# Kernel tuning notes

Hardware: AMD Instinct MI355X
Metric: run time of the kernel (lower is better)

Reference implementation:

```python
import jax, jax.numpy as jnp
import numpy as np

N = 512          # pedestrians in scene
T = 12           # decode steps
OBS = 8
FEAT = 2
LAT = 32
COND = 64
LSTM_IN = 128
HID = 64         # lstm_hidden_size == context_state_size
CTX = 64
EMB = 32         # Pooling_net spatial embedding dim
MLP_IN = EMB + 2 * CTX   # 160
MLP_MID = 64
BOT = CTX        # bottleneck_dim = h_dim
IN_DEC = COND + LAT + CTX + FEAT  # 162


def setup_inputs() -> dict:
    key = jax.random.key(0)
    ks = jax.random.split(key, 24)
    s = 0.1
    return {
        "last_position": jax.random.normal(ks[0], (N, FEAT), jnp.float32),
        "c": jax.random.normal(ks[1], (N, COND), jnp.float32),
        "z": jax.random.normal(ks[2], (N, LAT), jnp.float32),
        "obs_traj_pos": jax.random.normal(ks[3], (OBS, N, FEAT), jnp.float32),
        "nei_index": jax.random.randint(ks[4], (T, N, N), 0, 2, jnp.int32),
        "nei_num_index": jax.random.randint(ks[5], (N,), 0, N, jnp.int32),
        "h0": jax.random.normal(ks[6], (N, HID), jnp.float32),
        "c0": jax.random.normal(ks[7], (N, HID), jnp.float32),
        "eps": jax.random.normal(ks[8], (T, N, FEAT), jnp.float32),
        "W_in": jax.random.normal(ks[9], (IN_DEC, LSTM_IN), jnp.float32) * s,
        "b_in": jnp.zeros((LSTM_IN,), jnp.float32),
        "W_ih": jax.random.normal(ks[10], (4 * HID, LSTM_IN), jnp.float32) * s,
        "W_hh": jax.random.normal(ks[11], (4 * HID, HID), jnp.float32) * s,
        "b_ih": jnp.zeros((4 * HID,), jnp.float32),
        "b_hh": jnp.zeros((4 * HID,), jnp.float32),
        "W_l2p": jax.random.normal(ks[12], (HID // 2 + CTX, FEAT), jnp.float32) * s,
        "b_l2p": jnp.zeros((FEAT,), jnp.float32),
        "W_sp": jax.random.normal(ks[13], (FEAT, EMB), jnp.float32) * s,
        "b_sp": jnp.zeros((EMB,), jnp.float32),
        "W1": jax.random.normal(ks[14], (MLP_IN, MLP_MID), jnp.float32) * s,
        "b1": jnp.zeros((MLP_MID,), jnp.float32),
        "W2": jax.random.normal(ks[15], (MLP_MID, BOT), jnp.float32) * s,
        "b2": jnp.zeros((BOT,), jnp.float32),
    }


def reference(last_position, c, z, obs_traj_pos, nei_index, nei_num_index,
              h0, c0, eps, W_in, b_in, W_ih, W_hh, b_ih, b_hh,
              W_l2p, b_l2p, W_sp, b_sp, W1, b1, W2, b2):
    sg = jax.lax.stop_gradient
    half = HID // 2
    neg_inf = jnp.float32(-jnp.inf)

    def pooling(mask, lstm_state, pos):
        # mask: [N,N] bool; lstm_state: [N,CTX]; pos: [N,2]
        corr = pos[:, None, :] - pos[None, :, :]           # [N,N,2] pos[i]-pos[j]
        r = corr @ W_sp + b_sp                              # [N,N,EMB]
        hj = jnp.broadcast_to(lstm_state[None, :, :], (N, N, CTX))
        hi = jnp.broadcast_to(lstm_state[:, None, :], (N, N, CTX))
        x = jnp.concatenate([r, hj, hi], axis=-1)           # [N,N,160]
        h1 = jax.nn.relu(x @ W1 + b1)
        h2 = jax.nn.relu(h1 @ W2 + b2)                      # [N,N,BOT]
        Hm = jnp.where(mask[:, :, None], h2, neg_inf)       # scatter of valid rows
        pool = Hm.max(axis=1)                               # max over neighbors j
        return jnp.where(pool == neg_inf, 0.0, pool)

    def lstm_cell(x, h, cs):
        gates = x @ W_ih.T + b_ih + h @ W_hh.T + b_hh
        i, f, g, o = jnp.split(gates, 4, axis=-1)
        c_new = jax.nn.sigmoid(f) * cs + jax.nn.sigmoid(i) * jnp.tanh(g)
        h_new = jax.nn.sigmoid(o) * jnp.tanh(c_new)
        return h_new, c_new

    def step(carry, xs):
        prev_pos, h, cs, ctx, cur_abs = carry
        nei_t, eps_t = xs
        emb = jnp.concatenate([sg(prev_pos), sg(c), sg(z), sg(ctx)], axis=-1)
        x = jax.nn.relu(emb @ W_in + b_in)
        h, cs = lstm_cell(x, h, cs)
        ctx = pooling(nei_t > 0, h, cur_abs)
        mu = jnp.concatenate([h[:, :half], ctx], -1) @ W_l2p + b_l2p
        logvar = jnp.concatenate([h[:, half:], ctx], -1) @ W_l2p + b_l2p
        pos = mu + eps_t * jnp.exp(0.5 * logvar)
        cur_abs = sg(cur_abs + pos)
        return (pos, h, cs, ctx, cur_abs), (pos, mu, logvar)

    ctx0 = jnp.zeros((N, CTX), jnp.float32)
    carry0 = (last_position, h0, c0, ctx0, obs_traj_pos[-1])
    _, (pre_pos, mean, var) = jax.lax.scan(step, carry0, (nei_index, eps))
    return pre_pos, mean, var
```

## Files before the change

### kernel.cpp

```cpp
#include <hip/hip_runtime.h>
#include <math.h>

#define NP 512
#define TT 12

typedef float f32x4 __attribute__((ext_vector_type(4)));
typedef __bf16 bf16x8 __attribute__((ext_vector_type(8)));

#define OFF_CURABS 0
#define OFF_QB     2048
#define OFF_P      34816
#define OFF_H      67584
#define OFF_CS     100352
#define OFF_XCZ    133120
#define OFF_WGB    198656
#define OFF_WCTXB  223232
#define OFF_W1B    227328
#define OFF_WIN01  231424
#define OFF_WC     231680
#define OFF_BASE   231808
#define OFF_W2F    231872

__global__ __launch_bounds__(256) void init_k(
    const float* __restrict__ obs, const float* __restrict__ cc,
    const float* __restrict__ zz,
    const float* __restrict__ W_in, const float* __restrict__ W_ih,
    const float* __restrict__ W_hh, const float* __restrict__ W_sp,
    const float* __restrict__ b_sp, const float* __restrict__ W1,
    const float* __restrict__ b1, const float* __restrict__ W2,
    float* __restrict__ ws) {
  if (blockIdx.x < 128) {
    int id = blockIdx.x * 256 + threadIdx.x;
    if (id < 1024) ws[OFF_CURABS + id] = obs[7 * 1024 + id];
    __bf16* wgb = (__bf16*)(ws + OFF_WGB);
    for (int e = id; e < 49152; e += 32768) {
      int k = e >> 8, g = e & 255;
      float v = (k < 128) ? W_ih[g * 128 + k] : W_hh[g * 64 + (k - 128)];
      wgb[e] = (__bf16)v;
    }
    if (id < 8192) {
      int d = id >> 7, k = id & 127;
      ((__bf16*)(ws + OFF_WCTXB))[id] = (__bf16)W_in[(98 + d) * 128 + k];
    }
    if (id < 8192) {
      int r = id >> 6, m = id & 63;
      ((__bf16*)(ws + OFF_W1B))[id] = (__bf16)W1[(32 + r) * 64 + m];
    }
    if (id < 256) ws[OFF_WIN01 + id] = W_in[(id >> 7) * 128 + (id & 127)];
    if (id < 128) {
      int d = id >> 6, m = id & 63;
      float s = 0.f;
      for (int e = 0; e < 32; ++e) s = fmaf(W_sp[d * 32 + e], W1[e * 64 + m], s);
      ws[OFF_WC + id] = s;
    }
    if (id < 64) {
      float s = b1[id];
      for (int e = 0; e < 32; ++e) s = fmaf(b_sp[e], W1[e * 64 + id], s);
      ws[OFF_BASE + id] = s;
    }
    if (id < 4096) {
      int e = id & 7, f = (id >> 3) & 7, cq = id >> 6;
      int col = cq >> 2, quad = cq & 3, mt = f >> 1, kh = f & 1;
      ((__bf16*)(ws + OFF_W2F))[id] =
          (__bf16)W2[(kh * 32 + quad * 8 + e) * 64 + (mt * 16 + col)];
    }
  } else {
    int b = blockIdx.x - 128;
    int k = threadIdx.x;
    if (k < 128) {
      float s = 0.f;
      for (int d = 0; d < 64; ++d) s = fmaf(cc[b * 64 + d], W_in[(2 + d) * 128 + k], s);
      for (int d = 0; d < 32; ++d) s = fmaf(zz[b * 32 + d], W_in[(66 + d) * 128 + k], s);
      ws[OFF_XCZ + b * 128 + k] = s;
    }
  }
}

__global__ __launch_bounds__(256) void step_k(
    const float* __restrict__ lastpos, const int* __restrict__ nei,
    const float* __restrict__ h0, const float* __restrict__ c0,
    const float* __restrict__ obs, const float* __restrict__ epsin,
    const float* __restrict__ b_in,
    const float* __restrict__ b_ih, const float* __restrict__ b_hh,
    const float* __restrict__ Wl2p, const float* __restrict__ bl2p,
    const float* __restrict__ b2,
    float* __restrict__ out, float* __restrict__ ws, int s) {
  __shared__ int   ml[512];
  __shared__ float wcl[128], basev[64];
  __shared__ float red[4][64];
  __shared__ float hloc[64], csloc[64], ctxloc[64], prevp[2], pxy[2];
  __shared__ float xpart[2][128], xvec[128], gl[256];

  int t = threadIdx.x;
  int b = blockIdx.x;
  int lane = t & 63, w = t >> 6;
  int quad = lane >> 4, col = lane & 15;

  float pf = 0.f;
  if (s < TT) {
    const float* wsrc = ws + OFF_WGB;
    #pragma unroll
    for (int k = 0; k < 4; ++k) pf += wsrc[(t + k * 256) * 24];
  }

  if (t < 64) {
    if (s == 0) { hloc[t] = h0[b * 64 + t]; csloc[t] = c0[b * 64 + t]; ctxloc[t] = 0.f; }
    else        { hloc[t] = ws[OFF_H + b * 64 + t]; csloc[t] = ws[OFF_CS + b * 64 + t]; }
    basev[t] = ws[OFF_BASE + t];
  } else if (t < 192) {
    wcl[t - 64] = ws[OFF_WC + (t - 64)];
  }
  if (s == 0 && t < 2) {
    prevp[t] = lastpos[b * 2 + t];
    pxy[t]   = obs[7 * 1024 + b * 2 + t];
  }
  if (s > 0) {
    const int* neirow = nei + ((size_t)(s - 1) * NP + b) * NP;
    for (int j = t; j < 512; j += 256) ml[j] = neirow[j];
  }
  if (pf == 1.2345e-33f) ws[OFF_CURABS + 1] = pf;
  __syncthreads();

  if (s > 0) {
    int st = s - 1;
    const __bf16* Qb = (const __bf16*)(ws + OFF_QB) + (st & 1) * 32768;
    const __bf16* wf = (const __bf16*)(ws + OFF_W2F) + (col * 4 + quad) * 64;
    bf16x8 bf00 = *(const bf16x8*)&wf[0];
    bf16x8 bf01 = *(const bf16x8*)&wf[8];
    bf16x8 bf10 = *(const bf16x8*)&wf[16];
    bf16x8 bf11 = *(const bf16x8*)&wf[24];
    bf16x8 bf20 = *(const bf16x8*)&wf[32];
    bf16x8 bf21 = *(const bf16x8*)&wf[40];
    bf16x8 bf30 = *(const bf16x8*)&wf[48];
    bf16x8 bf31 = *(const bf16x8*)&wf[56];
    float pl0[8], pl1[8];
    #pragma unroll
    for (int e = 0; e < 8; ++e) {
      pl0[e] = ws[OFF_P + b * 64 + quad * 8 + e];
      pl1[e] = ws[OFF_P + b * 64 + 32 + quad * 8 + e];
    }
    float vmax0 = -1e30f, vmax1 = -1e30f, vmax2 = -1e30f, vmax3 = -1e30f;

    for (int c = 0; c < 8; ++c) {
      int j = w * 128 + c * 16 + col;
      bf16x8 q0 = *(const bf16x8*)&Qb[j * 64 + quad * 8];
      bf16x8 q1 = *(const bf16x8*)&Qb[j * 64 + 32 + quad * 8];
      bf16x8 a0, a1;
      #pragma unroll
      for (int e = 0; e < 8; ++e) {
        a0[e] = (__bf16)fmaxf((float)q0[e] + pl0[e], 0.f);
        a1[e] = (__bf16)fmaxf((float)q1[e] + pl1[e], 0.f);
      }
      int mrow = w * 128 + c * 16 + quad * 4;
      bool mk0 = ml[mrow] > 0, mk1 = ml[mrow + 1] > 0,
           mk2 = ml[mrow + 2] > 0, mk3 = ml[mrow + 3] > 0;
      f32x4 acc;
      acc = (f32x4){0.f, 0.f, 0.f, 0.f};
      acc = __builtin_amdgcn_mfma_f32_16x16x32_bf16(a0, bf00, acc, 0, 0, 0);
      acc = __builtin_amdgcn_mfma_f32_16x16x32_bf16(a1, bf01, acc, 0, 0, 0);
      vmax0 = fmaxf(vmax0, mk0 ? acc[0] : -1e30f);
      vmax0 = fmaxf(vmax0, mk1 ? acc[1] : -1e30f);
      vmax0 = fmaxf(vmax0, mk2 ? acc[2] : -1e30f);
      vmax0 = fmaxf(vmax0, mk3 ? acc[3] : -1e30f);
      acc = (f32x4){0.f, 0.f, 0.f, 0.f};
      acc = __builtin_amdgcn_mfma_f32_16x16x32_bf16(a0, bf10, acc, 0, 0, 0);
      acc = __builtin_amdgcn_mfma_f32_16x16x32_bf16(a1, bf11, acc, 0, 0, 0);
      vmax1 = fmaxf(vmax1, mk0 ? acc[0] : -1e30f);
      vmax1 = fmaxf(vmax1, mk1 ? acc[1] : -1e30f);
      vmax1 = fmaxf(vmax1, mk2 ? acc[2] : -1e30f);
      vmax1 = fmaxf(vmax1, mk3 ? acc[3] : -1e30f);
      acc = (f32x4){0.f, 0.f, 0.f, 0.f};
      acc = __builtin_amdgcn_mfma_f32_16x16x32_bf16(a0, bf20, acc, 0, 0, 0);
      acc = __builtin_amdgcn_mfma_f32_16x16x32_bf16(a1, bf21, acc, 0, 0, 0);
      vmax2 = fmaxf(vmax2, mk0 ? acc[0] : -1e30f);
      vmax2 = fmaxf(vmax2, mk1 ? acc[1] : -1e30f);
      vmax2 = fmaxf(vmax2, mk2 ? acc[2] : -1e30f);
      vmax2 = fmaxf(vmax2, mk3 ? acc[3] : -1e30f);
      acc = (f32x4){0.f, 0.f, 0.f, 0.f};
      acc = __builtin_amdgcn_mfma_f32_16x16x32_bf16(a0, bf30, acc, 0, 0, 0);
      acc = __builtin_amdgcn_mfma_f32_16x16x32_bf16(a1, bf31, acc, 0, 0, 0);
      vmax3 = fmaxf(vmax3, mk0 ? acc[0] : -1e30f);
      vmax3 = fmaxf(vmax3, mk1 ? acc[1] : -1e30f);
      vmax3 = fmaxf(vmax3, mk2 ? acc[2] : -1e30f);
      vmax3 = fmaxf(vmax3, mk3 ? acc[3] : -1e30f);
    }
    vmax0 = fmaxf(vmax0, __shfl_xor(vmax0, 16));
    vmax0 = fmaxf(vmax0, __shfl_xor(vmax0, 32));
    vmax1 = fmaxf(vmax1, __shfl_xor(vmax1, 16));
    vmax1 = fmaxf(vmax1, __shfl_xor(vmax1, 32));
    vmax2 = fmaxf(vmax2, __shfl_xor(vmax2, 16));
    vmax2 = fmaxf(vmax2, __shfl_xor(vmax2, 32));
    vmax3 = fmaxf(vmax3, __shfl_xor(vmax3, 16));
    vmax3 = fmaxf(vmax3, __shfl_xor(vmax3, 32));
    if (lane < 16) {
      red[w][0 * 16 + lane] = vmax0;
      red[w][1 * 16 + lane] = vmax1;
      red[w][2 * 16 + lane] = vmax2;
      red[w][3 * 16 + lane] = vmax3;
    }
    __syncthreads();
    if (t < 64) {
      float m4 = fmaxf(fmaxf(red[0][t], red[1][t]),
                       fmaxf(red[2][t], red[3][t]));
      ctxloc[t] = fmaxf(m4 + b2[t], 0.f);
    }
    __syncthreads();
    if (t < 64) {
      int l = t;
      float cl = ctxloc[l];
      float sc0 = cl * Wl2p[(32 + l) * 2 + 0];
      float sc1 = cl * Wl2p[(32 + l) * 2 + 1];
      float m0 = 0.f, m1 = 0.f, v0 = 0.f, v1 = 0.f;
      if (l < 32) {
        float hm = hloc[l];
        m0 = hm * Wl2p[l * 2 + 0]; m1 = hm * Wl2p[l * 2 + 1];
        float hv = hloc[32 + l];
        v0 = hv * Wl2p[l * 2 + 0]; v1 = hv * Wl2p[l * 2 + 1];
      }
      for (int off = 32; off >= 1; off >>= 1) {
        sc0 += __shfl_down(sc0, off);
        sc1 += __shfl_down(sc1, off);
        m0  += __shfl_down(m0,  off);
        m1  += __shfl_down(m1,  off);
        v0  += __shfl_down(v0,  off);
        v1  += __shfl_down(v1,  off);
      }
      if (l == 0) {
        float mu0 = m0 + sc0 + bl2p[0], mu1 = m1 + sc1 + bl2p[1];
        float lv0 = v0 + sc0 + bl2p[0], lv1 = v1 + sc1 + bl2p[1];
        float e0 = epsin[st * 1024 + b * 2 + 0];
        float e1 = epsin[st * 1024 + b * 2 + 1];
        float p0 = mu0 + e0 * expf(0.5f * lv0);
        float p1 = mu1 + e1 * expf(0.5f * lv1);
        out[st * 1024 + b * 2 + 0] = p0;
        out[st * 1024 + b * 2 + 1] = p1;
        out[12288 + st * 1024 + b * 2 + 0] = mu0;
        out[12288 + st * 1024 + b * 2 + 1] = mu1;
        out[24576 + st * 1024 + b * 2 + 0] = lv0;
        out[24576 + st * 1024 + b * 2 + 1] = lv1;
        float px = ws[OFF_CURABS + (st & 1) * 1024 + b * 2 + 0];
        float py = ws[OFF_CURABS + (st & 1) * 1024 + b * 2 + 1];
        float nx = px + p0, ny = py + p1;
        ws[OFF_CURABS + ((st & 1) ^ 1) * 1024 + b * 2 + 0] = nx;
        ws[OFF_CURABS + ((st & 1) ^ 1) * 1024 + b * 2 + 1] = ny;
        pxy[0] = nx; pxy[1] = ny;
        prevp[0] = p0; prevp[1] = p1;
      }
    }
    __syncthreads();
  }

  if (s < TT) {
    {
      int k = t & 127, p = t >> 7;
      const __bf16* wctx = (const __bf16*)(ws + OFF_WCTXB);
      float a0 = 0.f, a1 = 0.f;
      if (p == 0)
        a0 = ws[OFF_XCZ + b * 128 + k] +
             prevp[0] * ws[OFF_WIN01 + k] + prevp[1] * ws[OFF_WIN01 + 128 + k];
      int d = p;
      for (; d + 2 < 64; d += 4) {
        a0 = fmaf(ctxloc[d],     (float)wctx[d * 128 + k],       a0);
        a1 = fmaf(ctxloc[d + 2], (float)wctx[(d + 2) * 128 + k], a1);
      }
      if (d < 64) a0 = fmaf(ctxloc[d], (float)wctx[d * 128 + k], a0);
      xpart[p][k] = a0 + a1;
    }
    __syncthreads();
    if (t < 128) xvec[t] = fmaxf(xpart[0][t] + xpart[1][t] + b_in[t], 0.f);
    __syncthreads();
    {
      int g = t;
      const __bf16* wgb = (const __bf16*)(ws + OFF_WGB);
      float s0 = 0.f, s1 = 0.f, s2 = 0.f, s3 = 0.f;
      for (int kk = 0; kk < 128; kk += 4) {
        s0 = fmaf(xvec[kk],     (float)wgb[kk * 256 + g],       s0);
        s1 = fmaf(xvec[kk + 1], (float)wgb[(kk + 1) * 256 + g], s1);
        s2 = fmaf(xvec[kk + 2], (float)wgb[(kk + 2) * 256 + g], s2);
        s3 = fmaf(xvec[kk + 3], (float)wgb[(kk + 3) * 256 + g], s3);
      }
      for (int kk = 0; kk < 64; kk += 4) {
        s0 = fmaf(hloc[kk],     (float)wgb[(128 + kk) * 256 + g], s0);
        s1 = fmaf(hloc[kk + 1], (float)wgb[(129 + kk) * 256 + g], s1);
        s2 = fmaf(hloc[kk + 2], (float)wgb[(130 + kk) * 256 + g], s2);
        s3 = fmaf(hloc[kk + 3], (float)wgb[(131 + kk) * 256 + g], s3);
      }
      gl[g] = b_ih[g] + b_hh[g] + ((s0 + s1) + (s2 + s3));
    }
    __syncthreads();
    if (t < 64) {
      float ig = gl[t], fg = gl[64 + t], gg = gl[128 + t], og = gl[192 + t];
      float is = 1.f / (1.f + expf(-ig));
      float fs = 1.f / (1.f + expf(-fg));
      float os = 1.f / (1.f + expf(-og));
      float cn = fs * csloc[t] + is * tanhf(gg);
      float hv = os * tanhf(cn);
      hloc[t] = hv;
      ws[OFF_CS + b * 64 + t] = cn;
      ws[OFF_H + b * 64 + t] = hv;
    }
    __syncthreads();
    if (t < 128) {
      int which = t >> 6, m = t & 63;
      const __bf16* wb = (const __bf16*)(ws + OFF_W1B) + which * 4096 + m;
      float s0 = 0.f, s1 = 0.f, s2 = 0.f, s3 = 0.f;
      for (int k = 0; k < 64; k += 4) {
        s0 = fmaf(hloc[k],     (float)wb[k * 64],       s0);
        s1 = fmaf(hloc[k + 1], (float)wb[(k + 1) * 64], s1);
        s2 = fmaf(hloc[k + 2], (float)wb[(k + 2) * 64], s2);
        s3 = fmaf(hloc[k + 3], (float)wb[(k + 3) * 64], s3);
      }
      float sv = (s0 + s1) + (s2 + s3);
      float cx = pxy[0], cy = pxy[1];
      if (which == 0)
        ((__bf16*)(ws + OFF_QB))[(s & 1) * 32768 + b * 64 + m] =
            (__bf16)(sv + basev[m] - cx * wcl[m] - cy * wcl[64 + m]);
      else
        ws[OFF_P + b * 64 + m] = sv + cx * wcl[m] + cy * wcl[64 + m];
    }
  }
}

extern "C" void kernel_launch(void* const* d_in, const int* in_sizes, int n_in,
                              void* d_out, int out_size, void* d_ws, size_t ws_size,
                              hipStream_t stream) {
  const float* lastpos = (const float*)d_in[0];
  const float* cc      = (const float*)d_in[1];
  const float* zz      = (const float*)d_in[2];
  const float* obs     = (const float*)d_in[3];
  const int*   nei     = (const int*)d_in[4];
  const float* h0      = (const float*)d_in[6];
  const float* c0      = (const float*)d_in[7];
  const float* eps     = (const float*)d_in[8];
  const float* W_in    = (const float*)d_in[9];
  const float* b_in    = (const float*)d_in[10];
  const float* W_ih    = (const float*)d_in[11];
  const float* W_hh    = (const float*)d_in[12];
  const float* b_ih    = (const float*)d_in[13];
  const float* b_hh    = (const float*)d_in[14];
  const float* W_l2p   = (const float*)d_in[15];
  const float* b_l2p   = (const float*)d_in[16];
  const float* W_sp    = (const float*)d_in[17];
  const float* b_sp    = (const float*)d_in[18];
  const float* W1      = (const float*)d_in[19];
  const float* b1      = (const float*)d_in[20];
  const float* W2      = (const float*)d_in[21];
  const float* b2      = (const float*)d_in[22];
  float* out = (float*)d_out;
  float* ws  = (float*)d_ws;

  hipLaunchKernelGGL(init_k, dim3(640), dim3(256), 0, stream,
                     obs, cc, zz, W_in, W_ih, W_hh, W_sp, b_sp, W1, b1, W2, ws);
  for (int s = 0; s <= TT; ++s) {
    hipLaunchKernelGGL(step_k, dim3(NP), dim3(256), 0, stream,
                       lastpos, nei, h0, c0, obs, eps,
                       b_in, b_ih, b_hh, W_l2p, b_l2p,
                       b2, out, ws, s);
  }
}
```

Before: 336.8 us.

## Replace per-step kernel launches with persistent kernel and global atomic barrier

Replaces 13 separate step launches with a single persistent kernel of 64 blocks, each owning 8 pedestrians, that keeps h, c, ctx and positions in shared memory and syncs across blocks with an atomic counter barrier per step. Weight layouts are transposed for vectorized bf16 reads, and the Q matrix is streamed through double-buffered LDS tiles. This removes launch overhead and global state round-trips. In exchange it uses only 64 CUs, so each block computes the pooling over all 512 neighbours for 8 pedestrians, and the spin barrier relies on all blocks being co-resident.

Result: slower. 721.5 us (+114.2%).

```diff
diff --git a/kernel.cpp b/kernel.cpp
--- a/kernel.cpp
+++ b/kernel.cpp
@@ -3,27 +3,29 @@
 
 #define NP 512
 #define TT 12
+#define NB 64
 
 typedef float f32x4 __attribute__((ext_vector_type(4)));
 typedef __bf16 bf16x8 __attribute__((ext_vector_type(8)));
 
-#define OFF_CURABS 0
-#define OFF_QB     2048
-#define OFF_P      34816
-#define OFF_H      67584
-#define OFF_CS     100352
-#define OFF_XCZ    133120
-#define OFF_WGB    198656
-#define OFF_WCTXB  223232
-#define OFF_W1B    227328
-#define OFF_WIN01  231424
-#define OFF_WC     231680
-#define OFF_BASE   231808
-#define OFF_W2F    231872
+#define OFF_QB     0
+#define OFF_XCZ    32768
+#define OFF_WGT    98304
+#define OFF_WCTXT  122880
+#define OFF_W1T    126976
+#define OFF_WIN01  131072
+#define OFF_WC     131328
+#define OFF_BASE   131456
+#define OFF_W2F    131520
+#define OFF_BAR    133568
+
+#define AT_LD64(p)   __hip_atomic_load((p), __ATOMIC_RELAXED, __HIP_MEMORY_SCOPE_AGENT)
+#define AT_ST32(p,v) __hip_atomic_store((p), (v), __ATOMIC_RELAXED, __HIP_MEMORY_SCOPE_AGENT)
+
+union BU { __bf16 h; unsigned short u; };
 
 __global__ __launch_bounds__(256) void init_k(
-    const float* __restrict__ obs, const float* __restrict__ cc,
-    const float* __restrict__ zz,
+    const float* __restrict__ cc, const float* __restrict__ zz,
     const float* __restrict__ W_in, const float* __restrict__ W_ih,
     const float* __restrict__ W_hh, const float* __restrict__ W_sp,
     const float* __restrict__ b_sp, const float* __restrict__ W1,
@@ -31,20 +33,18 @@
     float* __restrict__ ws) {
   if (blockIdx.x < 128) {
     int id = blockIdx.x * 256 + threadIdx.x;
-    if (id < 1024) ws[OFF_CURABS + id] = obs[7 * 1024 + id];
-    __bf16* wgb = (__bf16*)(ws + OFF_WGB);
+    __bf16* wgt = (__bf16*)(ws + OFF_WGT);
     for (int e = id; e < 49152; e += 32768) {
-      int k = e >> 8, g = e & 255;
-      float v = (k < 128) ? W_ih[g * 128 + k] : W_hh[g * 64 + (k - 128)];
-      wgb[e] = (__bf16)v;
+      int g = e / 192, k = e - g * 192;
+      wgt[e] = (__bf16)((k < 128) ? W_ih[g * 128 + k] : W_hh[g * 64 + (k - 128)]);
     }
     if (id < 8192) {
-      int d = id >> 7, k = id & 127;
-      ((__bf16*)(ws + OFF_WCTXB))[id] = (__bf16)W_in[(98 + d) * 128 + k];
+      int k = id >> 6, d = id & 63;
+      ((__bf16*)(ws + OFF_WCTXT))[id] = (__bf16)W_in[(98 + d) * 128 + k];
     }
     if (id < 8192) {
-      int r = id >> 6, m = id & 63;
-      ((__bf16*)(ws + OFF_W1B))[id] = (__bf16)W1[(32 + r) * 64 + m];
+      int which = id >> 12, m = (id >> 6) & 63, k = id & 63;
+      ((__bf16*)(ws + OFF_W1T))[id] = (__bf16)W1[(32 + which * 64 + k) * 64 + m];
     }
     if (id < 256) ws[OFF_WIN01 + id] = W_in[(id >> 7) * 128 + (id & 127)];
     if (id < 128) {
@@ -64,6 +64,7 @@
       ((__bf16*)(ws + OFF_W2F))[id] =
           (__bf16)W2[(kh * 32 + quad * 8 + e) * 64 + (mt * 16 + col)];
     }
+    if (id < 16) ((int*)(ws + OFF_BAR))[id] = 0;
   } else {
     int b = blockIdx.x - 128;
     int k = threadIdx.x;
@@ -76,7 +77,7 @@
   }
 }
 
-__global__ __launch_bounds__(256) void step_k(
+__global__ __launch_bounds__(256) void persist_k(
     const float* __restrict__ lastpos, const int* __restrict__ nei,
     const float* __restrict__ h0, const float* __restrict__ c0,
     const float* __restrict__ obs, const float* __restrict__ epsin,
@@ -84,240 +85,314 @@
     const float* __restrict__ b_ih, const float* __restrict__ b_hh,
     const float* __restrict__ Wl2p, const float* __restrict__ bl2p,
     const float* __restrict__ b2,
-    float* __restrict__ out, float* __restrict__ ws, int s) {
-  __shared__ int   ml[512];
-  __shared__ float wcl[128], basev[64];
-  __shared__ float red[4][64];
-  __shared__ float hloc[64], csloc[64], ctxloc[64], prevp[2], pxy[2];
-  __shared__ float xpart[2][128], xvec[128], gl[256];
+    float* __restrict__ out, float* __restrict__ ws) {
+  __shared__ __align__(16) __bf16 Qc[2][64 * 72];
+  __shared__ __align__(16) float P8[8][64];
+  __shared__ __align__(16) float h8[8][64], cs8[8][64], ctx8[8][64];
+  __shared__ float prev8[8][2], pxy8[8][2];
+  __shared__ __align__(16) float xv2[2][128];
+  __shared__ float gl2[2][256];
+  __shared__ float basev[64], wcl[128];
 
   int t = threadIdx.x;
   int b = blockIdx.x;
   int lane = t & 63, w = t >> 6;
   int quad = lane >> 4, col = lane & 15;
-
-  float pf = 0.f;
-  if (s < TT) {
-    const float* wsrc = ws + OFF_WGB;
+  int* bar = (int*)(ws + OFF_BAR);
+  const __bf16* wgt   = (const __bf16*)(ws + OFF_WGT);
+  const __bf16* wctxT = (const __bf16*)(ws + OFF_WCTXT);
+  const __bf16* w1T   = (const __bf16*)(ws + OFF_W1T);
+
+  for (int e = t; e < 512; e += 256) {
+    int pp = e >> 6, u = e & 63;
+    h8[pp][u]  = h0[(b * 8 + pp) * 64 + u];
+    cs8[pp][u] = c0[(b * 8 + pp) * 64 + u];
+    ctx8[pp][u] = 0.f;
+  }
+  if (t < 16) {
+    int pp = t >> 1, d = t & 1;
+    prev8[pp][d] = lastpos[(b * 8 + pp) * 2 + d];
+    pxy8[pp][d]  = obs[7 * 1024 + (b * 8 + pp) * 2 + d];
+  }
+  if (t < 64) basev[t] = ws[OFF_BASE + t];
+  else if (t < 192) wcl[t - 64] = ws[OFF_WC + (t - 64)];
+  const __bf16* wf = (const __bf16*)(ws + OFF_W2F) + (col * 4 + quad) * 64;
+  bf16x8 bf00 = *(const bf16x8*)&wf[0];
+  bf16x8 bf01 = *(const bf16x8*)&wf[8];
+  bf16x8 bf10 = *(const bf16x8*)&wf[16];
+  bf16x8 bf11 = *(const bf16x8*)&wf[24];
+  bf16x8 bf20 = *(const bf16x8*)&wf[32];
+  bf16x8 bf21 = *(const bf16x8*)&wf[40];
+  bf16x8 bf30 = *(const bf16x8*)&wf[48];
+  bf16x8 bf31 = *(const bf16x8*)&wf[56];
+  __syncthreads();
+
+  for (int st = 0; st < TT; ++st) {
+    for (int pp2 = 0; pp2 < 4; ++pp2) {
+      int pa = pp2 * 2;
+      {
+        int pe = t >> 7, k = t & 127, lp = pa + pe, gp = b * 8 + lp;
+        float a0 = ws[OFF_XCZ + gp * 128 + k] + b_in[k] +
+                   prev8[lp][0] * ws[OFF_WIN01 + k] +
+                   prev8[lp][1] * ws[OFF_WIN01 + 128 + k];
+        const __bf16* wk = wctxT + k * 64;
+        float s0 = 0.f, s1 = 0.f;
+        #pragma unroll
+        for (int d = 0; d < 64; d += 8) {
+          bf16x8 wv = *(const bf16x8*)&wk[d];
+          f32x4 c0 = *(const f32x4*)&ctx8[lp][d];
+          f32x4 c1 = *(const f32x4*)&ctx8[lp][d + 4];
+          s0 = fmaf(c0[0], (float)wv[0], s0); s1 = fmaf(c0[1], (float)wv[1], s1);
+          s0 = fmaf(c0[2], (float)wv[2], s0); s1 = fmaf(c0[3], (float)wv[3], s1);
+          s0 = fmaf(c1[0], (float)wv[4], s0); s1 = fmaf(c1[1], (float)wv[5], s1);
+          s0 = fmaf(c1[2], (float)wv[6], s0); s1 = fmaf(c1[3], (float)wv[7], s1);
+        }
+        xv2[pe][k] = fmaxf(a0 + s0 + s1, 0.f);
+      }
+      __syncthreads();
+      {
+        int g = t;
+        const __bf16* wg = wgt + g * 192;
+        float biasg = b_ih[g] + b_hh[g];
+        float A0 = 0.f, A1 = 0.f, B0 = 0.f, B1 = 0.f;
+        #pragma unroll
+        for (int kk = 0; kk < 128; kk += 8) {
+          bf16x8 wv = *(const bf16x8*)&wg[kk];
+          f32x4 xa0 = *(const f32x4*)&xv2[0][kk];
+          f32x4 xa1 = *(const f32x4*)&xv2[0][kk + 4];
+          f32x4 xb0 = *(const f32x4*)&xv2[1][kk];
+          f32x4 xb1 = *(const f32x4*)&xv2[1][kk + 4];
+          #pragma unroll
+          for (int e = 0; e < 4; ++e) {
+            float wa = (float)wv[e], wb2 = (float)wv[e + 4];
+            A0 = fmaf(xa0[e], wa, A0); A1 = fmaf(xa1[e], wb2, A1);
+            B0 = fmaf(xb0[e], wa, B0); B1 = fmaf(xb1[e], wb2, B1);
+          }
+        }
+        #pragma unroll
+        for (int kk = 0; kk < 64; kk += 8) {
+          bf16x8 wv = *(const bf16x8*)&wg[128 + kk];
+          f32x4 ha0 = *(const f32x4*)&h8[pa][kk];
+          f32x4 ha1 = *(const f32x4*)&h8[pa][kk + 4];
+          f32x4 hb0 = *(const f32x4*)&h8[pa + 1][kk];
+          f32x4 hb1 = *(const f32x4*)&h8[pa + 1][kk + 4];
+          #pragma unroll
+          for (int e = 0; e < 4; ++e) {
+            float wa = (float)wv[e], wb2 = (float)wv[e + 4];
+            A0 = fmaf(ha0[e], wa, A0); A1 = fmaf(ha1[e], wb2, A1);
+            B0 = fmaf(hb0[e], wa, B0); B1 = fmaf(hb1[e], wb2, B1);
+          }
+        }
+        gl2[0][g] = biasg + A0 + A1;
+        gl2[1][g] = biasg + B0 + B1;
+      }
+      __syncthreads();
+      if (t < 128) {
+        int pe = t >> 6, u = t & 63, lp = pa + pe;
+        float ig = gl2[pe][u], fg = gl2[pe][64 + u];
+        float gg = gl2[pe][128 + u], og = gl2[pe][192 + u];
+        float is = 1.f / (1.f + expf(-ig));
+        float fs = 1.f / (1.f + expf(-fg));
+        float os = 1.f / (1.f + expf(-og));
+        float cn = fs * cs8[lp][u] + is * tanhf(gg);
+        cs8[lp][u] = cn;
+        h8[lp][u] = os * tanhf(cn);
+      }
+      __syncthreads();
+      {
+        int pe = t >> 7, which = (t >> 6) & 1, m = t & 63;
+        int lp = pa + pe, gp = b * 8 + lp;
+        const __bf16* wr = w1T + which * 4096 + m * 64;
+        float s0 = 0.f, s1 = 0.f;
+        #pragma unroll
+        for (int k = 0; k < 64; k += 8) {
+          bf16x8 wv = *(const bf16x8*)&wr[k];
+          f32x4 hv0 = *(const f32x4*)&h8[lp][k];
+          f32x4 hv1 = *(const f32x4*)&h8[lp][k + 4];
+          s0 = fmaf(hv0[0], (float)wv[0], s0); s1 = fmaf(hv0[1], (float)wv[1], s1);
+          s0 = fmaf(hv0[2], (float)wv[2], s0); s1 = fmaf(hv0[3], (float)wv[3], s1);
+          s0 = fmaf(hv1[0], (float)wv[4], s0); s1 = fmaf(hv1[1], (float)wv[5], s1);
+          s0 = fmaf(hv1[2], (float)wv[6], s0); s1 = fmaf(hv1[3], (float)wv[7], s1);
+        }
+        float sv = s0 + s1;
+        float px = pxy8[lp][0], py = pxy8[lp][1];
+        if (which == 0) {
+          float qv = sv + basev[m] - px * wcl[m] - py * wcl[64 + m];
+          float qlo = __shfl(qv, (lane << 1));
+          float qhi = __shfl(qv, (lane << 1) + 1);
+          if (lane < 32) {
+            BU ulo, uhi; ulo.h = (__bf16)qlo; uhi.h = (__bf16)qhi;
+            unsigned int u32 = ((unsigned int)uhi.u << 16) | ulo.u;
+            unsigned int* qdst =
+                (unsigned int*)((__bf16*)(ws + OFF_QB) + (st & 1) * 32768);
+            AT_ST32(qdst + gp * 32 + lane, u32);
+          }
+        } else {
+          P8[lp][m] = sv + px * wcl[m] + py * wcl[64 + m];
+        }
+      }
+    }
+
+    __syncthreads();
+    if (t == 0) {
+      __hip_atomic_fetch_add(&bar[st], 1, __ATOMIC_RELAXED, __HIP_MEMORY_SCOPE_AGENT);
+      while (__hip_atomic_load(&bar[st], __ATOMIC_RELAXED, __HIP_MEMORY_SCOPE_AGENT) < NB)
+        __builtin_amdgcn_s_sleep(2);
+    }
+    __syncthreads();
+
+    const unsigned long long* qsrc =
+        (const unsigned long long*)((__bf16*)(ws + OFF_QB) + (st & 1) * 32768);
+    int lpA = w * 2, lpB = w * 2 + 1;
+    int gpA = b * 8 + lpA, gpB = b * 8 + lpB;
+    const int* neiA = nei + ((size_t)st * NP + gpA) * NP;
+    const int* neiB = nei + ((size_t)st * NP + gpB) * NP;
+    float vmA0 = -1e30f, vmA1 = -1e30f, vmA2 = -1e30f, vmA3 = -1e30f;
+    float vmB0 = -1e30f, vmB1 = -1e30f, vmB2 = -1e30f, vmB3 = -1e30f;
+
+    unsigned long long v0, v1, v2, v3;
+    v0 = AT_LD64(qsrc + 0 * 256 + t); v1 = AT_LD64(qsrc + 1 * 256 + t);
+    v2 = AT_LD64(qsrc + 2 * 256 + t); v3 = AT_LD64(qsrc + 3 * 256 + t);
+    {
+      int f0 = t, f1 = 256 + t, f2 = 512 + t, f3 = 768 + t;
+      *(unsigned long long*)&Qc[0][(f0 >> 4) * 72 + (f0 & 15) * 4] = v0;
+      *(unsigned long long*)&Qc[0][(f1 >> 4) * 72 + (f1 & 15) * 4] = v1;
+      *(unsigned long long*)&Qc[0][(f2 >> 4) * 72 + (f2 & 15) * 4] = v2;
+      *(unsigned long long*)&Qc[0][(f3 >> 4) * 72 + (f3 & 15) * 4] = v3;
+    }
+    __syncthreads();
+
+    for (int c = 0; c < 8; ++c) {
+      int buf = c & 1;
+      if (c < 7) {
+        v0 = AT_LD64(qsrc + (c + 1) * 1024 + 0 * 256 + t);
+        v1 = AT_LD64(qsrc + (c + 1) * 1024 + 1 * 256 + t);
+        v2 = AT_LD64(qsrc + (c + 1) * 1024 + 2 * 256 + t);
+        v3 = AT_LD64(qsrc + (c + 1) * 1024 + 3 * 256 + t);
+      }
+      int mvA = neiA[c * 64 + lane];
+      int mvB = neiB[c * 64 + lane];
+      #pragma unroll
+      for (int ped = 0; ped < 2; ++ped) {
+        int lp = ped ? lpB : lpA;
+        int mv = ped ? mvB : mvA;
+        f32x4 pa0 = *(const f32x4*)&P8[lp][quad * 8];
+        f32x4 pa1 = *(const f32x4*)&P8[lp][quad * 8 + 4];
+        f32x4 pb0 = *(const f32x4*)&P8[lp][32 + quad * 8];
+        f32x4 pb1 = *(const f32x4*)&P8[lp][32 + quad * 8 + 4];
+        #pragma unroll
+        for (int jt = 0; jt < 4; ++jt) {
+          int jrow = jt * 16 + col;
+          bf16x8 q0 = *(const bf16x8*)&Qc[buf][jrow * 72 + quad * 8];
+          bf16x8 q1 = *(const bf16x8*)&Qc[buf][jrow * 72 + 32 + quad * 8];
+          bf16x8 a0, a1;
+          #pragma unroll
+          for (int e = 0; e < 4; ++e) {
+            a0[e]     = (__bf16)fmaxf((float)q0[e]     + pa0[e], 0.f);
+            a0[e + 4] = (__bf16)fmaxf((float)q0[e + 4] + pa1[e], 0.f);
+            a1[e]     = (__bf16)fmaxf((float)q1[e]     + pb0[e], 0.f);
+            a1[e + 4] = (__bf16)fmaxf((float)q1[e + 4] + pb1[e], 0.f);
+          }
+          int mrow = jt * 16 + quad * 4;
+          bool mk0 = __shfl(mv, mrow)     > 0;
+          bool mk1 = __shfl(mv, mrow + 1) > 0;
+          bool mk2 = __shfl(mv, mrow + 2) > 0;
+          bool mk3 = __shfl(mv, mrow + 3) > 0;
+          f32x4 acc;
+          float* vm0p = ped ? &vmB0 : &vmA0;
+          float* vm1p = ped ? &vmB1 : &vmA1;
+          float* vm2p = ped ? &vmB2 : &vmA2;
+          float* vm3p = ped ? &vmB3 : &vmA3;
+          acc = (f32x4){0.f, 0.f, 0.f, 0.f};
+          acc = __builtin_amdgcn_mfma_f32_16x16x32_bf16(a0, bf00, acc, 0, 0, 0);
+          acc = __builtin_amdgcn_mfma_f32_16x16x32_bf16(a1, bf01, acc, 0, 0, 0);
+          *vm0p = fmaxf(*vm0p, mk0 ? acc[0] : -1e30f);
+          *vm0p = fmaxf(*vm0p, mk1 ? acc[1] : -1e30f);
+          *vm0p = fmaxf(*vm0p, mk2 ? acc[2] : -1e30f);
+          *vm0p = fmaxf(*vm0p, mk3 ? acc[3] : -1e30f);
+          acc = (f32x4){0.f, 0.f, 0.f, 0.f};
+          acc = __builtin_amdgcn_mfma_f32_16x16x32_bf16(a0, bf10, acc, 0, 0, 0);
+          acc = __builtin_amdgcn_mfma_f32_16x16x32_bf16(a1, bf11, acc, 0, 0, 0);
+          *vm1p = fmaxf(*vm1p, mk0 ? acc[0] : -1e30f);
+          *vm1p = fmaxf(*vm1p, mk1 ? acc[1] : -1e30f);
+          *vm1p = fmaxf(*vm1p, mk2 ? acc[2] : -1e30f);
+          *vm1p = fmaxf(*vm1p, mk3 ? acc[3] : -1e30f);
+          acc = (f32x4){0.f, 0.f, 0.f, 0.f};
+          acc = __builtin_amdgcn_mfma_f32_16x16x32_bf16(a0, bf20, acc, 0, 0, 0);
+          acc = __builtin_amdgcn_mfma_f32_16x16x32_bf16(a1, bf21, acc, 0, 0, 0);
+          *vm2p = fmaxf(*vm2p, mk0 ? acc[0] : -1e30f);
+          *vm2p = fmaxf(*vm2p, mk1 ? acc[1] : -1e30f);
+          *vm2p = fmaxf(*vm2p, mk2 ? acc[2] : -1e30f);
+          *vm2p = fmaxf(*vm2p, mk3 ? acc[3] : -1e30f);
+          acc = (f32x4){0.f, 0.f, 0.f, 0.f};
+          acc = __builtin_amdgcn_mfma_f32_16x16x32_bf16(a0, bf30, acc, 0, 0, 0);
+          acc = __builtin_amdgcn_mfma_f32_16x16x32_bf16(a1, bf31, acc, 0, 0, 0);
+          *vm3p = fmaxf(*vm3p, mk0 ? acc[0] : -1e30f);
+          *vm3p = fmaxf(*vm3p, mk1 ? acc[1] : -1e30f);
+          *vm3p = fmaxf(*vm3p, mk2 ? acc[2] : -1e30f);
+          *vm3p = fmaxf(*vm3p, mk3 ? acc[3] : -1e30f);
+        }
+      }
+      if (c < 7) {
+        int nb = buf ^ 1;
+        int f0 = t, f1 = 256 + t, f2 = 512 + t, f3 = 768 + t;
+        *(unsigned long long*)&Qc[nb][(f0 >> 4) * 72 + (f0 & 15) * 4] = v0;
+        *(unsigned long long*)&Qc[nb][(f1 >> 4) * 72 + (f1 & 15) * 4] = v1;
+        *(unsigned long long*)&Qc[nb][(f2 >> 4) * 72 + (f2 & 15) * 4] = v2;
+        *(unsigned long long*)&Qc[nb][(f3 >> 4) * 72 + (f3 & 15) * 4] = v3;
+      }
+      __syncthreads();
+    }
+
     #pragma unroll
-    for (int k = 0; k < 4; ++k) pf += wsrc[(t + k * 256) * 24];
-  }
-
-  if (t < 64) {
-    if (s == 0) { hloc[t] = h0[b * 64 + t]; csloc[t] = c0[b * 64 + t]; ctxloc[t] = 0.f; }
-    else        { hloc[t] = ws[OFF_H + b * 64 + t]; csloc[t] = ws[OFF_CS + b * 64 + t]; }
-    basev[t] = ws[OFF_BASE + t];
-  } else if (t < 192) {
-    wcl[t - 64] = ws[OFF_WC + (t - 64)];
-  }
-  if (s == 0 && t < 2) {
-    prevp[t] = lastpos[b * 2 + t];
-    pxy[t]   = obs[7 * 1024 + b * 2 + t];
-  }
-  if (s > 0) {
-    const int* neirow = nei + ((size_t)(s - 1) * NP + b) * NP;
-    for (int j = t; j < 512; j += 256) ml[j] = neirow[j];
-  }
-  if (pf == 1.2345e-33f) ws[OFF_CURABS + 1] = pf;
-  __syncthreads();
-
-  if (s > 0) {
-    int st = s - 1;
-    const __bf16* Qb = (const __bf16*)(ws + OFF_QB) + (st & 1) * 32768;
-    const __bf16* wf = (const __bf16*)(ws + OFF_W2F) + (col * 4 + quad) * 64;
-    bf16x8 bf00 = *(const bf16x8*)&wf[0];
-    bf16x8 bf01 = *(const bf16x8*)&wf[8];
-    bf16x8 bf10 = *(const bf16x8*)&wf[16];
-    bf16x8 bf11 = *(const bf16x8*)&wf[24];
-    bf16x8 bf20 = *(const bf16x8*)&wf[32];
-    bf16x8 bf21 = *(const bf16x8*)&wf[40];
-    bf16x8 bf30 = *(const bf16x8*)&wf[48];
-    bf16x8 bf31 = *(const bf16x8*)&wf[56];
-    float pl0[8], pl1[8];
-    #pragma unroll
-    for (int e = 0; e < 8; ++e) {
-      pl0[e] = ws[OFF_P + b * 64 + quad * 8 + e];
-      pl1[e] = ws[OFF_P + b * 64 + 32 + quad * 8 + e];
-    }
-    float vmax0 = -1e30f, vmax1 = -1e30f, vmax2 = -1e30f, vmax3 = -1e30f;
-
-    for (int c = 0; c < 8; ++c) {
-      int j = w * 128 + c * 16 + col;
-      bf16x8 q0 = *(const bf16x8*)&Qb[j * 64 + quad * 8];
-      bf16x8 q1 = *(const bf16x8*)&Qb[j * 64 + 32 + quad * 8];
-      bf16x8 a0, a1;
-      #pragma unroll
-      for (int e = 0; e < 8; ++e) {
-        a0[e] = (__bf16)fmaxf((float)q0[e] + pl0[e], 0.f);
-        a1[e] = (__bf16)fmaxf((float)q1[e] + pl1[e], 0.f);
-      }
-      int mrow = w * 128 + c * 16 + quad * 4;
-      bool mk0 = ml[mrow] > 0, mk1 = ml[mrow + 1] > 0,
-           mk2 = ml[mrow + 2] > 0, mk3 = ml[mrow + 3] > 0;
-      f32x4 acc;
-      acc = (f32x4){0.f, 0.f, 0.f, 0.f};
-      acc = __builtin_amdgcn_mfma_f32_16x16x32_bf16(a0, bf00, acc, 0, 0, 0);
-      acc = __builtin_amdgcn_mfma_f32_16x16x32_bf16(a1, bf01, acc, 0, 0, 0);
-      vmax0 = fmaxf(vmax0, mk0 ? acc[0] : -1e30f);
-      vmax0 = fmaxf(vmax0, mk1 ? acc[1] : -1e30f);
-      vmax0 = fmaxf(vmax0, mk2 ? acc[2] : -1e30f);
-      vmax0 = fmaxf(vmax0, mk3 ? acc[3] : -1e30f);
-      acc = (f32x4){0.f, 0.f, 0.f, 0.f};
-      acc = __builtin_amdgcn_mfma_f32_16x16x32_bf16(a0, bf10, acc, 0, 0, 0);
-      acc = __builtin_amdgcn_mfma_f32_16x16x32_bf16(a1, bf11, acc, 0, 0, 0);
-      vmax1 = fmaxf(vmax1, mk0 ? acc[0] : -1e30f);
-      vmax1 = fmaxf(vmax1, mk1 ? acc[1] : -1e30f);
-      vmax1 = fmaxf(vmax1, mk2 ? acc[2] : -1e30f);
-      vmax1 = fmaxf(vmax1, mk3 ? acc[3] : -1e30f);
-      acc = (f32x4){0.f, 0.f, 0.f, 0.f};
-      acc = __builtin_amdgcn_mfma_f32_16x16x32_bf16(a0, bf20, acc, 0, 0, 0);
-      acc = __builtin_amdgcn_mfma_f32_16x16x32_bf16(a1, bf21, acc, 0, 0, 0);
-      vmax2 = fmaxf(vmax2, mk0 ? acc[0] : -1e30f);
-      vmax2 = fmaxf(vmax2, mk1 ? acc[1] : -1e30f);
-      vmax2 = fmaxf(vmax2, mk2 ? acc[2] : -1e30f);
-      vmax2 = fmaxf(vmax2, mk3 ? acc[3] : -1e30f);
-      acc = (f32x4){0.f, 0.f, 0.f, 0.f};
-      acc = __builtin_amdgcn_mfma_f32_16x16x32_bf16(a0, bf30, acc, 0, 0, 0);
-      acc = __builtin_amdgcn_mfma_f32_16x16x32_bf16(a1, bf31, acc, 0, 0, 0);
-      vmax3 = fmaxf(vmax3, mk0 ? acc[0] : -1e30f);
-      vmax3 = fmaxf(vmax3, mk1 ? acc[1] : -1e30f);
-      vmax3 = fmaxf(vmax3, mk2 ? acc[2] : -1e30f);
-      vmax3 = fmaxf(vmax3, mk3 ? acc[3] : -1e30f);
-    }
-    vmax0 = fmaxf(vmax0, __shfl_xor(vmax0, 16));
-    vmax0 = fmaxf(vmax0, __shfl_xor(vmax0, 32));
-    vmax1 = fmaxf(vmax1, __shfl_xor(vmax1, 16));
-    vmax1 = fmaxf(vmax1, __shfl_xor(vmax1, 32));
-    vmax2 = fmaxf(vmax2, __shfl_xor(vmax2, 16));
-    vmax2 = fmaxf(vmax2, __shfl_xor(vmax2, 32));
-    vmax3 = fmaxf(vmax3, __shfl_xor(vmax3, 16));
-    vmax3 = fmaxf(vmax3, __shfl_xor(vmax3, 32));
-    if (lane < 16) {
-      red[w][0 * 16 + lane] = vmax0;
-      red[w][1 * 16 + lane] = vmax1;
-      red[w][2 * 16 + lane] = vmax2;
-      red[w][3 * 16 + lane] = vmax3;
-    }
-    __syncthreads();
-    if (t < 64) {
-      float m4 = fmaxf(fmaxf(red[0][t], red[1][t]),
-                       fmaxf(red[2][t], red[3][t]));
-      ctxloc[t] = fmaxf(m4 + b2[t], 0.f);
-    }
-    __syncthreads();
-    if (t < 64) {
-      int l = t;
-      float cl = ctxloc[l];
-      float sc0 = cl * Wl2p[(32 + l) * 2 + 0];
-      float sc1 = cl * Wl2p[(32 + l) * 2 + 1];
-      float m0 = 0.f, m1 = 0.f, v0 = 0.f, v1 = 0.f;
+    for (int ped = 0; ped < 2; ++ped) {
+      int lp = ped ? lpB : lpA, gp = ped ? gpB : gpA;
+      float m0v = ped ? vmB0 : vmA0, m1v = ped ? vmB1 : vmA1;
+      float m2v = ped ? vmB2 : vmA2, m3v = ped ? vmB3 : vmA3;
+      m0v = fmaxf(m0v, __shfl_xor(m0v, 16)); m0v = fmaxf(m0v, __shfl_xor(m0v, 32));
+      m1v = fmaxf(m1v, __shfl_xor(m1v, 16)); m1v = fmaxf(m1v, __shfl_xor(m1v, 32));
+      m2v = fmaxf(m2v, __shfl_xor(m2v, 16)); m2v = fmaxf(m2v, __shfl_xor(m2v, 32));
+      m3v = fmaxf(m3v, __shfl_xor(m3v, 16)); m3v = fmaxf(m3v, __shfl_xor(m3v, 32));
+      int mt = lane >> 4;
+      float cval = (mt == 0) ? m0v : (mt == 1) ? m1v : (mt == 2) ? m2v : m3v;
+      cval = fmaxf(cval + b2[lane], 0.f);
+      ctx8[lp][lane] = cval;
+      int l = lane;
+      float sc0 = cval * Wl2p[(32 + l) * 2 + 0];
+      float sc1 = cval * Wl2p[(32 + l) * 2 + 1];
+      float e0s = 0.f, e1s = 0.f, f0s = 0.f, f1s = 0.f;
       if (l < 32) {
-        float hm = hloc[l];
-        m0 = hm * Wl2p[l * 2 + 0]; m1 = hm * Wl2p[l * 2 + 1];
-        float hv = hloc[32 + l];
-        v0 = hv * Wl2p[l * 2 + 0]; v1 = hv * Wl2p[l * 2 + 1];
+        float hm = h8[lp][l];
+        e0s = hm * Wl2p[l * 2 + 0]; e1s = hm * Wl2p[l * 2 + 1];
+        float hv = h8[lp][32 + l];
+        f0s = hv * Wl2p[l * 2 + 0]; f1s = hv * Wl2p[l * 2 + 1];
       }
       for (int off = 32; off >= 1; off >>= 1) {
         sc0 += __shfl_down(sc0, off);
         sc1 += __shfl_down(sc1, off);
-        m0  += __shfl_down(m0,  off);
-        m1  += __shfl_down(m1,  off);
-        v0  += __shfl_down(v0,  off);
-        v1  += __shfl_down(v1,  off);
+        e0s += __shfl_down(e0s, off);
+        e1s += __shfl_down(e1s, off);
+        f0s += __shfl_down(f0s, off);
+        f1s += __shfl_down(f1s, off);
       }
       if (l == 0) {
-        float mu0 = m0 + sc0 + bl2p[0], mu1 = m1 + sc1 + bl2p[1];
-        float lv0 = v0 + sc0 + bl2p[0], lv1 = v1 + sc1 + bl2p[1];
-        float e0 = epsin[st * 1024 + b * 2 + 0];
-        float e1 = epsin[st * 1024 + b * 2 + 1];
-        float p0 = mu0 + e0 * expf(0.5f * lv0);
-        float p1 = mu1 + e1 * expf(0.5f * lv1);
-        out[st * 1024 + b * 2 + 0] = p0;
-        out[st * 1024 + b * 2 + 1] = p1;
-        out[12288 + st * 1024 + b * 2 + 0] = mu0;
-        out[12288 + st * 1024 + b * 2 + 1] = mu1;
-        out[24576 + st * 1024 + b * 2 + 0] = lv0;
-        out[24576 + st * 1024 + b * 2 + 1] = lv1;
-        float px = ws[OFF_CURABS + (st & 1) * 1024 + b * 2 + 0];
-        float py = ws[OFF_CURABS + (st & 1) * 1024 + b * 2 + 1];
-        float nx = px + p0, ny = py + p1;
-        ws[OFF_CURABS + ((st & 1) ^ 1) * 1024 + b * 2 + 0] = nx;
-        ws[OFF_CURABS + ((st & 1) ^ 1) * 1024 + b * 2 + 1] = ny;
-        pxy[0] = nx; pxy[1] = ny;
-        prevp[0] = p0; prevp[1] = p1;
+        float mu0 = e0s + sc0 + bl2p[0], mu1 = e1s + sc1 + bl2p[1];
+        float lv0 = f0s + sc0 + bl2p[0], lv1 = f1s + sc1 + bl2p[1];
+        float ee0 = epsin[st * 1024 + gp * 2 + 0];
+        float ee1 = epsin[st * 1024 + gp * 2 + 1];
+        float p0 = mu0 + ee0 * expf(0.5f * lv0);
+        float p1 = mu1 + ee1 * expf(0.5f * lv1);
+        out[st * 1024 + gp * 2 + 0] = p0;
+        out[st * 1024 + gp * 2 + 1] = p1;
+        out[12288 + st * 1024 + gp * 2 + 0] = mu0;
+        out[12288 + st * 1024 + gp * 2 + 1] = mu1;
+        out[24576 + st * 1024 + gp * 2 + 0] = lv0;
+        out[24576 + st * 1024 + gp * 2 + 1] = lv1;
+        prev8[lp][0] = p0; prev8[lp][1] = p1;
+        pxy8[lp][0] += p0; pxy8[lp][1] += p1;
       }
     }
     __syncthreads();
-  }
-
-  if (s < TT) {
-    {
-      int k = t & 127, p = t >> 7;
-      const __bf16* wctx = (const __bf16*)(ws + OFF_WCTXB);
-      float a0 = 0.f, a1 = 0.f;
-      if (p == 0)
-        a0 = ws[OFF_XCZ + b * 128 + k] +
-             prevp[0] * ws[OFF_WIN01 + k] + prevp[1] * ws[OFF_WIN01 + 128 + k];
-      int d = p;
-      for (; d + 2 < 64; d += 4) {
-        a0 = fmaf(ctxloc[d],     (float)wctx[d * 128 + k],       a0);
-        a1 = fmaf(ctxloc[d + 2], (float)wctx[(d + 2) * 128 + k], a1);
-      }
-      if (d < 64) a0 = fmaf(ctxloc[d], (float)wctx[d * 128 + k], a0);
-      xpart[p][k] = a0 + a1;
-    }
-    __syncthreads();
-    if (t < 128) xvec[t] = fmaxf(xpart[0][t] + xpart[1][t] + b_in[t], 0.f);
-    __syncthreads();
-    {
-      int g = t;
-      const __bf16* wgb = (const __bf16*)(ws + OFF_WGB);
-      float s0 = 0.f, s1 = 0.f, s2 = 0.f, s3 = 0.f;
-      for (int kk = 0; kk < 128; kk += 4) {
-        s0 = fmaf(xvec[kk],     (float)wgb[kk * 256 + g],       s0);
-        s1 = fmaf(xvec[kk + 1], (float)wgb[(kk + 1) * 256 + g], s1);
-        s2 = fmaf(xvec[kk + 2], (float)wgb[(kk + 2) * 256 + g], s2);
-        s3 = fmaf(xvec[kk + 3], (float)wgb[(kk + 3) * 256 + g], s3);
-      }
-      for (int kk = 0; kk < 64; kk += 4) {
-        s0 = fmaf(hloc[kk],     (float)wgb[(128 + kk) * 256 + g], s0);
-        s1 = fmaf(hloc[kk + 1], (float)wgb[(129 + kk) * 256 + g], s1);
-        s2 = fmaf(hloc[kk + 2], (float)wgb[(130 + kk) * 256 + g], s2);
-        s3 = fmaf(hloc[kk + 3], (float)wgb[(131 + kk) * 256 + g], s3);
-      }
-      gl[g] = b_ih[g] + b_hh[g] + ((s0 + s1) + (s2 + s3));
-    }
-    __syncthreads();
-    if (t < 64) {
-      float ig = gl[t], fg = gl[64 + t], gg = gl[128 + t], og = gl[192 + t];
-      float is = 1.f / (1.f + expf(-ig));
-      float fs = 1.f / (1.f + expf(-fg));
-      float os = 1.f / (1.f + expf(-og));
-      float cn = fs * csloc[t] + is * tanhf(gg);
-      float hv = os * tanhf(cn);
-      hloc[t] = hv;
-      ws[OFF_CS + b * 64 + t] = cn;
-      ws[OFF_H + b * 64 + t] = hv;
-    }
-    __syncthreads();
-    if (t < 128) {
-      int which = t >> 6, m = t & 63;
-      const __bf16* wb = (const __bf16*)(ws + OFF_W1B) + which * 4096 + m;
-      float s0 = 0.f, s1 = 0.f, s2 = 0.f, s3 = 0.f;
-      for (int k = 0; k < 64; k += 4) {
-        s0 = fmaf(hloc[k],     (float)wb[k * 64],       s0);
-        s1 = fmaf(hloc[k + 1], (float)wb[(k + 1) * 64], s1);
-        s2 = fmaf(hloc[k + 2], (float)wb[(k + 2) * 64], s2);
-        s3 = fmaf(hloc[k + 3], (float)wb[(k + 3) * 64], s3);
-      }
-      float sv = (s0 + s1) + (s2 + s3);
-      float cx = pxy[0], cy = pxy[1];
-      if (which == 0)
-        ((__bf16*)(ws + OFF_QB))[(s & 1) * 32768 + b * 64 + m] =
-            (__bf16)(sv + basev[m] - cx * wcl[m] - cy * wcl[64 + m]);
-      else
-        ws[OFF_P + b * 64 + m] = sv + cx * wcl[m] + cy * wcl[64 + m];
-    }
   }
 }
 
@@ -350,11 +425,8 @@
   float* ws  = (float*)d_ws;
 
   hipLaunchKernelGGL(init_k, dim3(640), dim3(256), 0, stream,
-                     obs, cc, zz, W_in, W_ih, W_hh, W_sp, b_sp, W1, b1, W2, ws);
-  for (int s = 0; s <= TT; ++s) {
-    hipLaunchKernelGGL(step_k, dim3(NP), dim3(256), 0, stream,
-                       lastpos, nei, h0, c0, obs, eps,
-                       b_in, b_ih, b_hh, W_l2p, b_l2p,
-                       b2, out, ws, s);
-  }
+                     cc, zz, W_in, W_ih, W_hh, W_sp, b_sp, W1, b1, W2, ws);
+  hipLaunchKernelGGL(persist_k, dim3(NB), dim3(256), 0, stream,
+                     lastpos, nei, h0, c0, obs, eps,
+                     b_in, b_ih, b_hh, W_l2p, b_l2p, b2, out, ws);
 }
```
